# Kernel optimization log

Measured on AMD Instinct MI355X. Metric: run time of the kernel, lower is better.

## Reference

```python
import jax, jax.numpy as jnp
import numpy as np

B, SEQ, C, H = 4, 1024, 256, 4
Dk = C // H                                  # 64
L = 4 * SEQ                                  # 4096 attention length
FACTOR = 4
N_TOP = FACTOR * int(np.ceil(np.log(L)))     # U = 36 dominant queries
SAMPLE_K = FACTOR * int(np.ceil(np.log(L)))  # u = 36 sampled keys per query


def _forward(et, mp, co, vol, Wq, bq, Wk, bk, Wv, bv, Wo, bo, index_sample):
    sz = et.shape[0]
    # student_graph input shuffle (faithful to the torch .view calls)
    x = jnp.concatenate([et.reshape(SEQ, -1), co.reshape(SEQ, -1),
                         mp.reshape(SEQ, -1), vol.reshape(SEQ, -1)], axis=-1)
    x = x.reshape(sz, L, C)  # [B, 4*seq_len, d_model]
    # projections; ProbAttention uses view(B,H,L,-1) which is a raw reshape
    # (NOT a transpose) of the [B,L,H,Dk] tensor -> fuse into one reshape
    q = (x @ Wq + bq).reshape(sz, H, L, Dk)
    k = (x @ Wk + bk).reshape(sz, H, L, Dk)
    v = (x @ Wv + bv).reshape(sz, H, L, Dk)
    # _prob_QK: random key sampling + sparsity measure + top-k query select
    K_sample = k[:, :, index_sample, :]                        # [B,H,L,u,Dk]
    QKs = jnp.einsum('bhse,bhske->bhsk', q, K_sample)          # [B,H,L,u]
    M = QKs.max(axis=-1) - QKs.sum(axis=-1) / L                # [B,H,L]
    _, m_top = jax.lax.top_k(M, N_TOP)                         # [B,H,U]
    q_red = jnp.take_along_axis(q, m_top[..., None], axis=2)   # [B,H,U,Dk]
    scores = jnp.einsum('bhue,bhle->bhul', q_red, k) * (1.0 / float(np.sqrt(Dk)))
    attn = jax.nn.softmax(scores, axis=-1)                     # [B,H,U,L]
    upd = jnp.einsum('bhul,bhld->bhud', attn, v)               # [B,H,U,Dk]
    # initial context = V-sum broadcast; scatter dense update at top queries
    ctx = jnp.broadcast_to(v.sum(axis=2, keepdims=True), (sz, H, L, Dk))
    bi = jnp.arange(sz)[:, None, None]
    hi = jnp.arange(H)[None, :, None]
    ctx = ctx.at[bi, hi, m_top, :].set(upd)                    # [B,H,L,Dk]
    # AttentionLayer output: .view(B, L, -1) on contiguous [B,H,L,Dk] is again
    # a raw reshape (faithful), then out projection
    out = ctx.reshape(sz, L, H * Dk) @ Wo + bo                 # [B,L,C]
    return out.reshape(SEQ, -1)


def setup_inputs():
    key = jax.random.key(0)
    ks = jax.random.split(key, 13)
    f = lambda i, shp: jax.random.normal(ks[i], shp, jnp.float32)
    ws = 1.0 / float(np.sqrt(C))  # keep logits in a sane range
    return {
        'et': f(0, (B, SEQ, C)), 'mp': f(1, (B, SEQ, C)),
        'co': f(2, (B, SEQ, C)), 'vol': f(3, (B, SEQ, C)),
        'Wq': f(4, (C, C)) * ws, 'bq': f(5, (C,)) * 0.01,
        'Wk': f(6, (C, C)) * ws, 'bk': f(7, (C,)) * 0.01,
        'Wv': f(8, (C, C)) * ws, 'bv': f(9, (C,)) * 0.01,
        'Wo': f(10, (C, C)) * ws, 'bo': f(11, (C,)) * 0.01,
        'index_sample': jax.random.randint(ks[12], (L, SAMPLE_K), 0, L, dtype=jnp.int32),
        'comp_idx': 0,
    }


def reference(et, mp, co, vol, Wq, bq, Wk, bk, Wv, bv, Wo, bo, index_sample, comp_idx):
    return _forward(et, mp, co, vol, Wq, bq, Wk, bk, Wv, bv, Wo, bo, index_sample)
```

## Files before the change

kernel.cpp:

```cpp
#include <hip/hip_runtime.h>
#include <hip/hip_bf16.h>

#define BHn 16
#define Ln 4096
#define NTOP 36
#define SKn 36
#define NCHUNK 64

using s16x8 = __attribute__((ext_vector_type(8))) short;
using u16x8 = __attribute__((ext_vector_type(8))) unsigned short;
using f32x4 = __attribute__((ext_vector_type(4))) float;

__device__ __forceinline__ unsigned short bf_hi(float f) {
  unsigned u = __float_as_uint(f);
  return (unsigned short)((u + 0x7fffu + ((u >> 16) & 1u)) >> 16);
}

__global__ __launch_bounds__(256) void wxconv(
    const float* __restrict__ W0, const float* __restrict__ W1, const float* __restrict__ W2,
    unsigned short* __restrict__ th0, unsigned short* __restrict__ tl0,
    unsigned short* __restrict__ th1, unsigned short* __restrict__ tl1,
    unsigned short* __restrict__ th2, unsigned short* __restrict__ tl2,
    const float* __restrict__ s0, const float* __restrict__ s1,
    const float* __restrict__ s2, const float* __restrict__ s3,
    unsigned short* __restrict__ Axh, unsigned short* __restrict__ Axl) {
  int bx = blockIdx.x;
  int t = threadIdx.x;
  if (bx < 48) {
    int wsel = bx >> 4;
    const float* W = (wsel == 0) ? W0 : (wsel == 1) ? W1 : W2;
    unsigned short* TH = (wsel == 0) ? th0 : (wsel == 1) ? th1 : th2;
    unsigned short* TL = (wsel == 0) ? tl0 : (wsel == 1) ? tl1 : tl2;
    int kr = (bx & 15) * 16;
    int n = t;
    u16x8 hv[2], lv[2];
#pragma unroll
    for (int j = 0; j < 16; ++j) {
      float f = W[(size_t)(kr + j) * 256 + n];
      unsigned short h = bf_hi(f);
      float lof = f - __uint_as_float(((unsigned)h) << 16);
      hv[j >> 3][j & 7] = h;
      lv[j >> 3][j & 7] = bf_hi(lof);
    }
    *(u16x8*)&TH[(size_t)n * 256 + kr] = hv[0];
    *(u16x8*)&TH[(size_t)n * 256 + kr + 8] = hv[1];
    *(u16x8*)&TL[(size_t)n * 256 + kr] = lv[0];
    *(u16x8*)&TL[(size_t)n * 256 + kr + 8] = lv[1];
  } else {
    int row = (bx - 48) * 4 + (t >> 6);
    int c = t & 63;
    int l = row & 4095, b = row >> 12;
    int part = (l >> 2) & 3;
    int seq = ((l >> 4) << 2) | (l & 3);
    const float* sp = (part == 0) ? s0 : (part == 1) ? s1 : (part == 2) ? s2 : s3;
    float4 f = ((const float4*)(sp + (size_t)((b << 10) + seq) * 256))[c];
    float fv[4] = {f.x, f.y, f.z, f.w};
    ushort4 hv, lv;
    unsigned short* hp = (unsigned short*)&hv;
    unsigned short* lp = (unsigned short*)&lv;
#pragma unroll
    for (int j = 0; j < 4; ++j) {
      unsigned short h = bf_hi(fv[j]);
      float lof = fv[j] - __uint_as_float(((unsigned)h) << 16);
      hp[j] = h;
      lp[j] = bf_hi(lof);
    }
    *(ushort4*)&Axh[(size_t)row * 256 + c * 4] = hv;
    *(ushort4*)&Axl[(size_t)row * 256 + c * 4] = lv;
  }
}

#define LDW 40
__global__ __launch_bounds__(256, 3) void qkv_mfma(
    const unsigned short* __restrict__ Axh, const unsigned short* __restrict__ Axl,
    const unsigned short* __restrict__ th0, const unsigned short* __restrict__ tl0,
    const unsigned short* __restrict__ th1, const unsigned short* __restrict__ tl1,
    const unsigned short* __restrict__ th2, const unsigned short* __restrict__ tl2,
    const float* __restrict__ b0, const float* __restrict__ b1, const float* __restrict__ b2,
    float* __restrict__ o0, float* __restrict__ o1, float* __restrict__ o2) {
  __shared__ __align__(16) unsigned short Ah[128 * LDW];
  __shared__ __align__(16) unsigned short Al[128 * LDW];
  __shared__ __align__(16) unsigned short Bh[128 * LDW];
  __shared__ __align__(16) unsigned short Bl[128 * LDW];
  int t = threadIdx.x;
  int g = blockIdx.x;
  int vnt = g >> 7;
  int wsel = vnt >> 1;
  int col0 = (vnt & 1) * 128;
  int row0 = (g & 127) * 128;
  const unsigned short* TH = (wsel == 0) ? th0 : (wsel == 1) ? th1 : th2;
  const unsigned short* TL = (wsel == 0) ? tl0 : (wsel == 1) ? tl1 : tl2;
  const float* bias = (wsel == 0) ? b0 : (wsel == 1) ? b1 : b2;
  float* O = (wsel == 0) ? o0 : (wsel == 1) ? o1 : o2;
  const bool vlite = (wsel == 2);

  int srow = t >> 1, half = t & 1;
  const unsigned short* ah_g = Axh + (size_t)(row0 + srow) * 256 + half * 16;
  const unsigned short* al_g = Axl + (size_t)(row0 + srow) * 256 + half * 16;
  const unsigned short* bh_g = TH + (size_t)(col0 + srow) * 256 + half * 16;
  const unsigned short* bl_g = TL + (size_t)(col0 + srow) * 256 + half * 16;

  int lane = t & 63;
  int wv = t >> 6;
  int wr = wv >> 1, wc = wv & 1;
  int fr = lane & 15, fk = lane >> 4;
  int aoff = (wr * 64 + fr) * LDW + fk * 8;
  int boff = (wc * 64 + fr) * LDW + fk * 8;

  f32x4 acc[4][4] = {};

  for (int k0 = 0; k0 < 256; k0 += 32) {
    int wa = srow * LDW + half * 16;
    u16x8 va0 = *(const u16x8*)(ah_g + k0);
    u16x8 va1 = *(const u16x8*)(ah_g + k0 + 8);
    u16x8 vb0 = *(const u16x8*)(bh_g + k0);
    u16x8 vb1 = *(const u16x8*)(bh_g + k0 + 8);
    *(u16x8*)&Ah[wa] = va0; *(u16x8*)&Ah[wa + 8] = va1;
    *(u16x8*)&Bh[wa] = vb0; *(u16x8*)&Bh[wa + 8] = vb1;
    if (!vlite) {
      u16x8 vl0 = *(const u16x8*)(al_g + k0);
      u16x8 vl1 = *(const u16x8*)(al_g + k0 + 8);
      u16x8 vc0 = *(const u16x8*)(bl_g + k0);
      u16x8 vc1 = *(const u16x8*)(bl_g + k0 + 8);
      *(u16x8*)&Al[wa] = vl0; *(u16x8*)&Al[wa + 8] = vl1;
      *(u16x8*)&Bl[wa] = vc0; *(u16x8*)&Bl[wa + 8] = vc1;
    }
    __syncthreads();

    if (vlite) {
      s16x8 fah[4];
#pragma unroll
      for (int mi = 0; mi < 4; ++mi)
        fah[mi] = *(const s16x8*)&Ah[aoff + mi * 16 * LDW];
#pragma unroll
      for (int ni = 0; ni < 4; ++ni) {
        s16x8 fbh = *(const s16x8*)&Bh[boff + ni * 16 * LDW];
#pragma unroll
        for (int mi = 0; mi < 4; ++mi)
          acc[mi][ni] = __builtin_amdgcn_mfma_f32_16x16x32_bf16(fah[mi], fbh, acc[mi][ni], 0, 0, 0);
      }
    } else {
      s16x8 fah[4], fal[4];
#pragma unroll
      for (int mi = 0; mi < 4; ++mi) {
        fah[mi] = *(const s16x8*)&Ah[aoff + mi * 16 * LDW];
        fal[mi] = *(const s16x8*)&Al[aoff + mi * 16 * LDW];
      }
#pragma unroll
      for (int ni = 0; ni < 4; ++ni) {
        s16x8 fbh = *(const s16x8*)&Bh[boff + ni * 16 * LDW];
        s16x8 fbl = *(const s16x8*)&Bl[boff + ni * 16 * LDW];
#pragma unroll
        for (int mi = 0; mi < 4; ++mi) {
          acc[mi][ni] = __builtin_amdgcn_mfma_f32_16x16x32_bf16(fah[mi], fbh, acc[mi][ni], 0, 0, 0);
          acc[mi][ni] = __builtin_amdgcn_mfma_f32_16x16x32_bf16(fal[mi], fbh, acc[mi][ni], 0, 0, 0);
          acc[mi][ni] = __builtin_amdgcn_mfma_f32_16x16x32_bf16(fah[mi], fbl, acc[mi][ni], 0, 0, 0);
        }
      }
    }
    __syncthreads();
  }

#pragma unroll
  for (int ni = 0; ni < 4; ++ni) {
    int n = col0 + wc * 64 + ni * 16 + fr;
    float bv = bias[n];
#pragma unroll
    for (int mi = 0; mi < 4; ++mi) {
      int mb = row0 + wr * 64 + mi * 16 + fk * 4;
#pragma unroll
      for (int r = 0; r < 4; ++r)
        O[(size_t)(mb + r) * 256 + n] = acc[mi][ni][r] + bv;
    }
  }
}

__global__ __launch_bounds__(256) void qks_m3(
    const float* __restrict__ q, const float* __restrict__ k,
    const int* __restrict__ idxs, float* __restrict__ Mout) {
  __shared__ float qs[64][68];
  __shared__ int il[64 * SKn];
  int g = blockIdx.x;
  int x = g & 7;
  int i = g >> 3;
  int bh = (x << 1) | (i >> 6);
  int s0 = (i & 63) * 64;
  int t = threadIdx.x;
  size_t base = (size_t)bh << 12;
  for (int i2 = t; i2 < 1024; i2 += 256) {
    int row = i2 >> 4, d4 = i2 & 15;
    *(float4*)&qs[row][d4 * 4] = ((const float4*)(q + (base + s0 + row) * 64))[d4];
  }
  for (int i2 = t; i2 < 64 * SKn; i2 += 256) il[i2] = idxs[s0 * SKn + i2];
  __syncthreads();
  int sl = t >> 2;
  int dq = t & 3;
  float qr[16];
#pragma unroll
  for (int i2 = 0; i2 < 4; ++i2)
    *(float4*)&qr[i2 * 4] = *(const float4*)&qs[sl][i2 * 16 + dq * 4];
  float mx = -INFINITY, sm = 0.f;
  const float4* kb4 = (const float4*)(k + base * 64);
#pragma unroll 4
  for (int j = 0; j < SKn; ++j) {
    int l = il[sl * SKn + j];
    const float4* kr = kb4 + (size_t)l * 16;
    float acc = 0.f;
#pragma unroll
    for (int i2 = 0; i2 < 4; ++i2) {
      float4 kv = kr[i2 * 4 + dq];
      acc += kv.x * qr[i2 * 4] + kv.y * qr[i2 * 4 + 1] + kv.z * qr[i2 * 4 + 2] + kv.w * qr[i2 * 4 + 3];
    }
    acc += __shfl_xor(acc, 1, 64);
    acc += __shfl_xor(acc, 2, 64);
    mx = fmaxf(mx, acc);
    sm += acc;
  }
  if (dq == 0) Mout[base + s0 + sl] = mx - sm * (1.0f / 4096.0f);
}

__global__ __launch_bounds__(256) void topk_radix(
    const float* __restrict__ M, int* __restrict__ topidx) {
  __shared__ unsigned hist[4096];
  __shared__ unsigned sup[256];
  __shared__ unsigned cand_u[256];
  __shared__ int cand_i[256];
  __shared__ int s_bin1, s_bin2, s_above, s_ocnt, s_ccnt;
  int bh = blockIdx.x;
  int t = threadIdx.x;
  int mbase = bh * 4096;
  unsigned uv[16];
  for (int i = t; i < 4096; i += 256) hist[i] = 0;
  __syncthreads();
#pragma unroll
  for (int r = 0; r < 16; ++r) {
    unsigned b = __float_as_uint(M[mbase + t + 256 * r]);
    unsigned u = b ^ ((unsigned)((int)b >> 31) | 0x80000000u);
    uv[r] = u;
    atomicAdd(&hist[u >> 20], 1u);
  }
  __syncthreads();
  {
    unsigned ssum = 0;
    for (int i = 0; i < 16; ++i) ssum += hist[t * 16 + i];
    sup[t] = ssum;
  }
  __syncthreads();
  if (t == 0) {
    unsigned cum = 0; int sb = 255;
    for (; sb > 0; --sb) { if (cum + sup[sb] >= NTOP) break; cum += sup[sb]; }
    int b = sb * 16 + 15;
    for (; b > sb * 16; --b) { if (cum + hist[b] >= NTOP) break; cum += hist[b]; }
    s_bin1 = b; s_above = (int)cum;
  }
  __syncthreads();
  int bin1 = s_bin1;
  int need1 = NTOP - s_above;
  __syncthreads();
  for (int i = t; i < 4096; i += 256) hist[i] = 0;
  __syncthreads();
#pragma unroll
  for (int r = 0; r < 16; ++r)
    if ((int)(uv[r] >> 20) == bin1) atomicAdd(&hist[(uv[r] >> 8) & 0xFFF], 1u);
  __syncthreads();
  {
    unsigned ssum = 0;
    for (int i = 0; i < 16; ++i) ssum += hist[t * 16 + i];
    sup[t] = ssum;
  }
  __syncthreads();
  if (t == 0) {
    unsigned cum = 0; int sb = 255;
    for (; sb > 0; --sb) { if (cum + sup[sb] >= (unsigned)need1) break; cum += sup[sb]; }
    int b = sb * 16 + 15;
    for (; b > sb * 16; --b) { if (cum + hist[b] >= (unsigned)need1) break; cum += hist[b]; }
    s_bin2 = b; s_above += (int)cum;
    s_ocnt = 0; s_ccnt = 0;
  }
  __syncthreads();
  int bin2 = s_bin2;
  int need = NTOP - s_above;
  int* outp = topidx + bh * NTOP;
#pragma unroll
  for (int r = 0; r < 16; ++r) {
    unsigned u = uv[r];
    int b1 = u >> 20, b2 = (u >> 8) & 0xFFF;
    if (b1 > bin1 || (b1 == bin1 && b2 > bin2)) {
      int p = atomicAdd(&s_ocnt, 1);
      outp[p] = t + 256 * r;
    } else if (b1 == bin1 && b2 == bin2) {
      int p = atomicAdd(&s_ccnt, 1);
      if (p < 256) { cand_u[p] = u; cand_i[p] = t + 256 * r; }
    }
  }
  __syncthreads();
  if (t == 0) {
    int cc = s_ccnt < 256 ? s_ccnt : 256;
    int slot = s_ocnt;
    for (int n = 0; n < need; ++n) {
      unsigned bu = 0; int bi = 0x7fffffff, bp = -1;
      for (int c = 0; c < cc; ++c) {
        if (cand_i[c] < 0) continue;
        if (cand_u[c] > bu || (cand_u[c] == bu && cand_i[c] < bi)) {
          bu = cand_u[c]; bi = cand_i[c]; bp = c;
        }
      }
      outp[slot++] = bi;
      cand_i[bp] = -1;
    }
  }
}

__global__ __launch_bounds__(256) void attn_partial(
    const float* __restrict__ q, const float* __restrict__ k,
    const float* __restrict__ v, const int* __restrict__ topidx,
    float* __restrict__ part_m, float* __restrict__ part_s,
    unsigned short* __restrict__ part_ob, float* __restrict__ vpart2) {
  __shared__ float4 Ks4[64][17];
  __shared__ float4 qs4[36][17];
  __shared__ float S[36][68];
  int g = blockIdx.x;
  int x = g & 7;
  int i = g >> 3;
  int bh = (x << 1) | (i >> 6);
  int c = i & 63;
  int l0 = c * 64;
  int t = threadIdx.x;
  size_t base = (size_t)bh * 4096;

  const float4* kg = (const float4*)(k + (base + l0) * 64);
  for (int i2 = t; i2 < 64 * 16; i2 += 256) {
    int row = i2 >> 4, d4 = i2 & 15;
    Ks4[row][d4] = kg[row * 16 + d4];
  }
  for (int i2 = t; i2 < 36 * 16; i2 += 256) {
    int u = i2 >> 4, d4 = i2 & 15;
    int m = topidx[bh * NTOP + u];
    qs4[u][d4] = ((const float4*)(q + (base + m) * 64))[d4];
  }
  __syncthreads();

  {
    int l = t & 63, ug = t >> 6;
    float acc[9] = {};
#pragma unroll
    for (int d4 = 0; d4 < 16; ++d4) {
      float4 kv = Ks4[l][d4];
#pragma unroll
      for (int j = 0; j < 9; ++j) {
        float4 qv = qs4[ug * 9 + j][d4];
        acc[j] += kv.x * qv.x + kv.y * qv.y + kv.z * qv.z + kv.w * qv.w;
      }
    }
#pragma unroll
    for (int j = 0; j < 9; ++j) S[ug * 9 + j][l] = acc[j] * 0.125f;
  }
  __syncthreads();

  if (t < 144) {
    int u = t >> 2, p = t & 3;
    int lb = p * 16;
    float mx = -INFINITY;
#pragma unroll
    for (int l2 = 0; l2 < 16; ++l2) mx = fmaxf(mx, S[u][lb + l2]);
    mx = fmaxf(mx, __shfl_xor(mx, 1, 64));
    mx = fmaxf(mx, __shfl_xor(mx, 2, 64));
    float sm = 0.f;
#pragma unroll
    for (int l2 = 0; l2 < 16; ++l2) {
      float e = expf(S[u][lb + l2] - mx);
      S[u][lb + l2] = e;
      sm += e;
    }
    sm += __shfl_xor(sm, 1, 64);
    sm += __shfl_xor(sm, 2, 64);
    if (p == 0) {
      part_m[((size_t)bh * NCHUNK + c) * NTOP + u] = mx;
      part_s[((size_t)bh * NCHUNK + c) * NTOP + u] = sm;
    }
  }
  __syncthreads();

  {
    int d = t & 63, ug = t >> 6;
    float pacc[9] = {};
    float vs = 0.f;
    const float* vg = v + (base + l0) * 64;
    for (int l = 0; l < 64; ++l) {
      float vv = vg[l * 64 + d];
      vs += vv;
#pragma unroll
      for (int j = 0; j < 9; ++j) pacc[j] += S[ug * 9 + j][l] * vv;
    }
#pragma unroll
    for (int j = 0; j < 9; ++j)
      part_ob[(((size_t)bh * NCHUNK + c) * NTOP + ug * 9 + j) * 64 + d] = bf_hi(pacc[j]);
    if (ug == 0) vpart2[((size_t)bh * NCHUNK + c) * 64 + d] = vs;
  }
}

__global__ __launch_bounds__(256) void vsum_out(
    const float* __restrict__ vpart2, const float* __restrict__ Wo,
    const float* __restrict__ bo, float* __restrict__ vsum,
    float* __restrict__ outbase) {
  __shared__ float red[4][64];
  __shared__ float vs[64];
  int bh = blockIdx.x;
  int t = threadIdx.x;
  int d = t & 63, qq = t >> 6;
  float acc = 0.f;
  for (int c = qq; c < NCHUNK; c += 4)
    acc += vpart2[((size_t)bh * NCHUNK + c) * 64 + d];
  red[qq][d] = acc;
  __syncthreads();
  if (qq == 0) {
    float s = red[0][d] + red[1][d] + red[2][d] + red[3][d];
    vs[d] = s;
    vsum[bh * 64 + d] = s;
  }
  __syncthreads();
  float ob = bo[t];
#pragma unroll 8
  for (int dd = 0; dd < 64; ++dd) {
    float w4 = Wo[dd * 256 + t] + Wo[(64 + dd) * 256 + t] +
               Wo[(128 + dd) * 256 + t] + Wo[(192 + dd) * 256 + t];
    ob += vs[dd] * w4;
  }
  outbase[bh * 256 + t] = ob;
}

__global__ __launch_bounds__(256) void out_fill(
    const float* __restrict__ outbase, float4* __restrict__ out4) {
  int g = blockIdx.x * 256 + threadIdx.x;
  int c4 = g & 63;
  int bh = g >> 16;
  out4[g] = ((const float4*)outbase)[bh * 64 + c4];
}

__global__ __launch_bounds__(256) void combine_patch(
    const float* __restrict__ part_m, const float* __restrict__ part_s,
    const unsigned short* __restrict__ part_ob, const float* __restrict__ vsum,
    const int* __restrict__ topidx, const float* __restrict__ Wo,
    float* __restrict__ out) {
  __shared__ float wl[64];
  __shared__ float red[4][64];
  __shared__ float dv[64];
  __shared__ float ds_s;
  int widx = blockIdx.x;
  int bh = widx / NTOP;
  int u = widx % NTOP;
  int t = threadIdx.x;
  int d = t & 63, qq = t >> 6;
  if (t < 64) {
    float m_c = part_m[((size_t)bh * NCHUNK + t) * NTOP + u];
    float M = m_c;
#pragma unroll
    for (int off = 32; off > 0; off >>= 1) M = fmaxf(M, __shfl_xor(M, off, 64));
    float w = expf(m_c - M);
    float ds = part_s[((size_t)bh * NCHUNK + t) * NTOP + u] * w;
#pragma unroll
    for (int off = 32; off > 0; off >>= 1) ds += __shfl_xor(ds, off, 64);
    wl[t] = w;
    if (t == 0) ds_s = ds;
  }
  __syncthreads();
  float acc = 0.f;
#pragma unroll
  for (int j = 0; j < 16; ++j) {
    int c = qq + j * 4;
    float po = __uint_as_float(
        ((unsigned)part_ob[(((size_t)bh * NCHUNK + c) * NTOP + u) * 64 + d]) << 16);
    acc += po * wl[c];
  }
  red[qq][d] = acc;
  __syncthreads();
  if (qq == 0)
    dv[d] = (red[0][d] + red[1][d] + red[2][d] + red[3][d]) / ds_s - vsum[bh * 64 + d];
  __syncthreads();
  int m = topidx[widx];
  int h = bh & 3, b = bh >> 2;
  int j2 = m & 3;
  int lp = h * 1024 + (m >> 2);
  float acc2 = 0.f;
#pragma unroll 8
  for (int dd = 0; dd < 64; ++dd) acc2 += dv[dd] * Wo[(j2 * 64 + dd) * 256 + t];
  atomicAdd(&out[((size_t)(b * 4096 + lp)) * 256 + t], acc2);
}

extern "C" void kernel_launch(void* const* d_in, const int* in_sizes, int n_in,
                              void* d_out, int out_size, void* d_ws, size_t ws_size,
                              hipStream_t stream) {
  const float* et  = (const float*)d_in[0];
  const float* mp  = (const float*)d_in[1];
  const float* co  = (const float*)d_in[2];
  const float* vol = (const float*)d_in[3];
  const float* Wq = (const float*)d_in[4];
  const float* bq = (const float*)d_in[5];
  const float* Wk = (const float*)d_in[6];
  const float* bk = (const float*)d_in[7];
  const float* Wv = (const float*)d_in[8];
  const float* bv = (const float*)d_in[9];
  const float* Wo = (const float*)d_in[10];
  const float* bo = (const float*)d_in[11];
  const int* idxs = (const int*)d_in[12];
  float* out = (float*)d_out;

  char* ws = (char*)d_ws;
  const size_t BIG = 16u * 1024u * 1024u;
  float* qb = (float*)(ws);
  float* kb = (float*)(ws + BIG);
  float* vb = (float*)(ws + 2 * BIG);
  char* sm = ws + 3 * BIG;
  float* Mbuf   = (float*)(sm);
  int*   topidx = (int*)(sm + 262144);
  float* vsum   = (float*)(sm + 262144 + 4096);
  char* pm = sm + 262144 + 4096 + 8192;
  float* part_m = (float*)(pm);
  float* part_s = (float*)(pm + 147456);
  unsigned short* part_ob = (unsigned short*)(pm + 2 * 147456);
  float* outbase = (float*)(pm + 2 * 147456 + 4718592);
  unsigned short* wt = (unsigned short*)(pm + 2 * 147456 + 4718592 + 16384);
  unsigned short* wth0 = wt;
  unsigned short* wtl0 = wt + 65536;
  unsigned short* wth1 = wt + 2 * 65536;
  unsigned short* wtl1 = wt + 3 * 65536;
  unsigned short* wth2 = wt + 4 * 65536;
  unsigned short* wtl2 = wt + 5 * 65536;
  unsigned short* axh = wt + 6 * 65536;
  unsigned short* axl = axh + 16384 * 256;
  float* vpart2 = (float*)(axl + 16384 * 256);

  wxconv<<<4144, 256, 0, stream>>>(Wq, Wk, Wv, wth0, wtl0, wth1, wtl1, wth2, wtl2,
                                   et, co, mp, vol, axh, axl);

  qkv_mfma<<<768, 256, 0, stream>>>(
      axh, axl, wth0, wtl0, wth1, wtl1, wth2, wtl2, bq, bk, bv, qb, kb, vb);

  qks_m3<<<1024, 256, 0, stream>>>(qb, kb, idxs, Mbuf);

  topk_radix<<<BHn, 256, 0, stream>>>(Mbuf, topidx);

  attn_partial<<<1024, 256, 0, stream>>>(
      qb, kb, vb, topidx, part_m, part_s, part_ob, vpart2);

  vsum_out<<<BHn, 256, 0, stream>>>(vpart2, Wo, bo, vsum, outbase);

  out_fill<<<4096, 256, 0, stream>>>(outbase, (float4*)out);

  combine_patch<<<BHn * NTOP, 256, 0, stream>>>(
      part_m, part_s, part_ob, vsum, topidx, Wo, out);
}
```

Measured before the change: 127.4 us.

## Stage QKV GEMM tiles via direct global-to-LDS loads with XOR-swizzled layout

```diff
diff --git a/kernel.cpp b/kernel.cpp
--- a/kernel.cpp
+++ b/kernel.cpp
@@ -14,6 +14,10 @@
 __device__ __forceinline__ unsigned short bf_hi(float f) {
   unsigned u = __float_as_uint(f);
   return (unsigned short)((u + 0x7fffu + ((u >> 16) & 1u)) >> 16);
+}
+
+__device__ __forceinline__ unsigned swz(unsigned a) {
+  return a ^ (((a >> 7) & 7) << 4);
 }
 
 __global__ __launch_bounds__(256) void wxconv(
@@ -70,7 +74,6 @@
   }
 }
 
-#define LDW 40
 __global__ __launch_bounds__(256, 3) void qkv_mfma(
     const unsigned short* __restrict__ Axh, const unsigned short* __restrict__ Axl,
     const unsigned short* __restrict__ th0, const unsigned short* __restrict__ tl0,
@@ -78,10 +81,10 @@
     const unsigned short* __restrict__ th2, const unsigned short* __restrict__ tl2,
     const float* __restrict__ b0, const float* __restrict__ b1, const float* __restrict__ b2,
     float* __restrict__ o0, float* __restrict__ o1, float* __restrict__ o2) {
-  __shared__ __align__(16) unsigned short Ah[128 * LDW];
-  __shared__ __align__(16) unsigned short Al[128 * LDW];
-  __shared__ __align__(16) unsigned short Bh[128 * LDW];
-  __shared__ __align__(16) unsigned short Bl[128 * LDW];
+  __shared__ __align__(16) unsigned short Ah[128 * 32];
+  __shared__ __align__(16) unsigned short Al[128 * 32];
+  __shared__ __align__(16) unsigned short Bh[128 * 32];
+  __shared__ __align__(16) unsigned short Bl[128 * 32];
   int t = threadIdx.x;
   int g = blockIdx.x;
   int vnt = g >> 7;
@@ -94,36 +97,43 @@
   float* O = (wsel == 0) ? o0 : (wsel == 1) ? o1 : o2;
   const bool vlite = (wsel == 2);
 
-  int srow = t >> 1, half = t & 1;
-  const unsigned short* ah_g = Axh + (size_t)(row0 + srow) * 256 + half * 16;
-  const unsigned short* al_g = Axl + (size_t)(row0 + srow) * 256 + half * 16;
-  const unsigned short* bh_g = TH + (size_t)(col0 + srow) * 256 + half * 16;
-  const unsigned short* bl_g = TL + (size_t)(col0 + srow) * 256 + half * 16;
-
   int lane = t & 63;
   int wv = t >> 6;
   int wr = wv >> 1, wc = wv & 1;
   int fr = lane & 15, fk = lane >> 4;
-  int aoff = (wr * 64 + fr) * LDW + fk * 8;
-  int boff = (wc * 64 + fr) * LDW + fk * 8;
+
+  const unsigned short* stage_src =
+      (wv == 0) ? Axh + (size_t)row0 * 256 :
+      (wv == 1) ? Axl + (size_t)row0 * 256 :
+      (wv == 2) ? TH + (size_t)col0 * 256 :
+                  TL + (size_t)col0 * 256;
+  unsigned short* stage_dst = (wv == 0) ? Ah : (wv == 1) ? Al : (wv == 2) ? Bh : Bl;
+  const bool stage_skip = vlite && (wv & 1);
+
+  unsigned offs[8];
+#pragma unroll
+  for (int i = 0; i < 8; ++i) {
+    unsigned phys = i * 1024 + lane * 16;
+    unsigned logical = swz(phys);
+    offs[i] = (logical >> 6) * 256 + ((logical & 63) >> 1);
+  }
+
+  unsigned aoffb[4], boffb[4];
+#pragma unroll
+  for (int mi = 0; mi < 4; ++mi) {
+    aoffb[mi] = swz((unsigned)((wr * 64 + mi * 16 + fr) * 64 + fk * 16));
+    boffb[mi] = swz((unsigned)((wc * 64 + mi * 16 + fr) * 64 + fk * 16));
+  }
 
   f32x4 acc[4][4] = {};
 
   for (int k0 = 0; k0 < 256; k0 += 32) {
-    int wa = srow * LDW + half * 16;
-    u16x8 va0 = *(const u16x8*)(ah_g + k0);
-    u16x8 va1 = *(const u16x8*)(ah_g + k0 + 8);
-    u16x8 vb0 = *(const u16x8*)(bh_g + k0);
-    u16x8 vb1 = *(const u16x8*)(bh_g + k0 + 8);
-    *(u16x8*)&Ah[wa] = va0; *(u16x8*)&Ah[wa + 8] = va1;
-    *(u16x8*)&Bh[wa] = vb0; *(u16x8*)&Bh[wa + 8] = vb1;
-    if (!vlite) {
-      u16x8 vl0 = *(const u16x8*)(al_g + k0);
-      u16x8 vl1 = *(const u16x8*)(al_g + k0 + 8);
-      u16x8 vc0 = *(const u16x8*)(bl_g + k0);
-      u16x8 vc1 = *(const u16x8*)(bl_g + k0 + 8);
-      *(u16x8*)&Al[wa] = vl0; *(u16x8*)&Al[wa + 8] = vl1;
-      *(u16x8*)&Bl[wa] = vc0; *(u16x8*)&Bl[wa + 8] = vc1;
+    if (!stage_skip) {
+#pragma unroll
+      for (int i = 0; i < 8; ++i)
+        __builtin_amdgcn_global_load_lds(
+            (const unsigned int*)(stage_src + offs[i] + k0),
+            (unsigned int*)((char*)stage_dst + i * 1024), 16, 0, 0);
     }
     __syncthreads();
 
@@ -131,10 +141,10 @@
       s16x8 fah[4];
 #pragma unroll
       for (int mi = 0; mi < 4; ++mi)
-        fah[mi] = *(const s16x8*)&Ah[aoff + mi * 16 * LDW];
+        fah[mi] = *(const s16x8*)((const char*)Ah + aoffb[mi]);
 #pragma unroll
       for (int ni = 0; ni < 4; ++ni) {
-        s16x8 fbh = *(const s16x8*)&Bh[boff + ni * 16 * LDW];
+        s16x8 fbh = *(const s16x8*)((const char*)Bh + boffb[ni]);
 #pragma unroll
         for (int mi = 0; mi < 4; ++mi)
           acc[mi][ni] = __builtin_amdgcn_mfma_f32_16x16x32_bf16(fah[mi], fbh, acc[mi][ni], 0, 0, 0);
@@ -143,13 +153,13 @@
       s16x8 fah[4], fal[4];
 #pragma unroll
       for (int mi = 0; mi < 4; ++mi) {
-        fah[mi] = *(const s16x8*)&Ah[aoff + mi * 16 * LDW];
-        fal[mi] = *(const s16x8*)&Al[aoff + mi * 16 * LDW];
+        fah[mi] = *(const s16x8*)((const char*)Ah + aoffb[mi]);
+        fal[mi] = *(const s16x8*)((const char*)Al + aoffb[mi]);
       }
 #pragma unroll
       for (int ni = 0; ni < 4; ++ni) {
-        s16x8 fbh = *(const s16x8*)&Bh[boff + ni * 16 * LDW];
-        s16x8 fbl = *(const s16x8*)&Bl[boff + ni * 16 * LDW];
+        s16x8 fbh = *(const s16x8*)((const char*)Bh + boffb[ni]);
+        s16x8 fbl = *(const s16x8*)((const char*)Bl + boffb[ni]);
 #pragma unroll
         for (int mi = 0; mi < 4; ++mi) {
           acc[mi][ni] = __builtin_amdgcn_mfma_f32_16x16x32_bf16(fah[mi], fbh, acc[mi][ni], 0, 0, 0);
```

After: 135.3 us. 1.06x slower.
